# Kernel optimization log

Measured on AMD Instinct MI355X. Metric: run time of the kernel, lower is better.

## Reference

```python
import jax, jax.numpy as jnp
import numpy as np

DIM = 3072
HEADS = 24
HEAD_DIM = DIM // HEADS  # 128
B, L = 2, 2048


def setup_inputs() -> dict:
    key = jax.random.key(0)
    ks = jax.random.split(key, 6)
    x = jax.random.normal(ks[0], (B, L, DIM), dtype=jnp.float32)
    # Build a genuine rotary freqs_cis tensor: [1,1,L,D/2,2,2]
    half = HEAD_DIM // 2
    inv_freq = 1.0 / (10000.0 ** (jnp.arange(0, half, dtype=jnp.float32) / half))
    ang = jnp.arange(L, dtype=jnp.float32)[:, None] * inv_freq[None, :]  # [L, D/2]
    cos, sin = jnp.cos(ang), jnp.sin(ang)
    # rotation matrix [[cos, -sin],[sin, cos]] stacked on last two dims
    pe = jnp.stack(
        [jnp.stack([cos, -sin], axis=-1), jnp.stack([sin, cos], axis=-1)], axis=-2
    )  # [L, D/2, 2, 2]
    pe = pe[None, None]  # [1,1,L,D/2,2,2]
    Wqkv = jax.random.normal(ks[1], (3 * DIM, DIM), dtype=jnp.float32) * 0.02
    bqkv = jax.random.normal(ks[2], (3 * DIM,), dtype=jnp.float32) * 0.02
    q_scale = jnp.ones((HEAD_DIM,), dtype=jnp.float32)
    k_scale = jnp.ones((HEAD_DIM,), dtype=jnp.float32)
    Wproj = jax.random.normal(ks[3], (DIM, DIM), dtype=jnp.float32) * 0.02
    bproj = jax.random.normal(ks[4], (DIM,), dtype=jnp.float32) * 0.02
    return {"x": x, "pe": pe, "Wqkv": Wqkv, "bqkv": bqkv,
            "q_scale": q_scale, "k_scale": k_scale,
            "Wproj": Wproj, "bproj": bproj}


def _rms_norm(t, scale):
    # computed in fp32 like the torch module (eps=1e-6)
    rrms = jax.lax.rsqrt(jnp.mean(t * t, axis=-1, keepdims=True) + 1e-6)
    return t * rrms * scale


def _apply_rope(t, pe):
    # t: [B,H,L,D]; pe: [1,1,L,D/2,2,2]
    b, h, l, d = t.shape
    t2 = t.reshape(b, h, l, d // 2, 1, 2)
    out = pe[..., 0] * t2[..., 0] + pe[..., 1] * t2[..., 1]  # [B,H,L,D/2,2]
    return out.reshape(b, h, l, d)


def reference(x, pe, Wqkv, bqkv, q_scale, k_scale, Wproj, bproj):
    b, l, dim = x.shape
    d = q_scale.shape[0]
    h = dim // d
    qkv = x @ Wqkv.T + bqkv                       # [B,L,3*dim]
    qkv = qkv.reshape(b, l, 3, h, d)
    q, k, v = jnp.transpose(qkv, (2, 0, 3, 1, 4))  # each [B,H,L,D]
    q = _rms_norm(q, q_scale)
    k = _rms_norm(k, k_scale)
    q = _apply_rope(q, pe)
    k = _apply_rope(k, pe)
    scale = 1.0 / jnp.sqrt(jnp.float32(d))
    scores = jnp.einsum("bhqd,bhkd->bhqk", q, k) * scale
    attn = jax.nn.softmax(scores, axis=-1)
    out = jnp.einsum("bhqk,bhkd->bhqd", attn, v)  # [B,H,L,D]
    out = jnp.transpose(out, (0, 2, 1, 3)).reshape(b, l, h * d)
    return out @ Wproj.T + bproj
```

## Files before the change

### kernel.cpp

```cpp
#include <hip/hip_runtime.h>

#define DIM   3072
#define HEADS 24
#define HDIM  128
#define BB    2
#define LSEQ  2048
#define BL    4096
#define NQKV  9216

typedef __bf16 bf16;
typedef __bf16 bf16x8 __attribute__((ext_vector_type(8)));
typedef float  f32x4  __attribute__((ext_vector_type(4)));

__device__ __forceinline__ void async_cp16(void* lds, const void* gp) {
  __builtin_amdgcn_global_load_lds(
      (const __attribute__((address_space(1))) void*)gp,
      (__attribute__((address_space(3))) void*)lds, 16, 0, 0);
}

__global__ void sniff_dtype(const unsigned short* __restrict__ w, int* __restrict__ flag) {
  if (threadIdx.x == 0 && blockIdx.x == 0) {
    int big = 0;
    for (int i = 0; i < 64; ++i) {
      const int e = (w[i] >> 7) & 0xFF;
      if (e >= 127) ++big;
    }
    *flag = (big >= 4) ? 1 : 0;
  }
}

__global__ __launch_bounds__(256) void to_bf16(
    const void* __restrict__ src, bf16* __restrict__ dst, long n,
    const int* __restrict__ flag) {
  const bool f = (*flag != 0);
  long i = (long)blockIdx.x * blockDim.x + threadIdx.x;
  const long stride = (long)gridDim.x * blockDim.x;
  if (f) {
    const float* s = (const float*)src;
    for (; i < n; i += stride) dst[i] = (bf16)s[i];
  } else {
    const unsigned short* s = (const unsigned short*)src;
    unsigned short* d = (unsigned short*)dst;
    for (; i < n; i += stride) d[i] = s[i];
  }
}

__global__ __launch_bounds__(256) void gemm_bt_bias(
    const bf16* __restrict__ A, const bf16* __restrict__ Bw,
    const bf16* __restrict__ bias, void* __restrict__ Cv,
    int M, int N, int K, const int* __restrict__ flag)
{
  __shared__ bf16 As[128*32];
  __shared__ bf16 Bs[128*32];
  const bool f32out = (flag != nullptr) && (*flag != 0);
  const int tid  = threadIdx.x;
  const int wave = tid >> 6, lane = tid & 63;
  const int bm = blockIdx.x * 128, bn = blockIdx.y * 128;
  const int wm = (wave >> 1) * 64, wn = (wave & 1) * 64;
  const int lm = lane & 15, q8 = (lane >> 4) * 8;
  const int rsub = lane >> 2;
  const int cb   = (lane & 3) * 16;

  const f32x4 zero4 = {0.f, 0.f, 0.f, 0.f};
  f32x4 acc[4][4];
  for (int i = 0; i < 4; ++i)
    for (int j = 0; j < 4; ++j) acc[i][j] = zero4;

  for (int k0 = 0; k0 < K; k0 += 32) {
    #pragma unroll
    for (int j = 0; j < 2; ++j) {
      const int r = wave*32 + j*16 + rsub;
      async_cp16((char*)As + r*64 + cb,
                 (const char*)(A + (size_t)(bm + r)*K + k0) + cb);
      async_cp16((char*)Bs + r*64 + cb,
                 (const char*)(Bw + (size_t)(bn + r)*K + k0) + cb);
    }
    __syncthreads();
    bf16x8 af[4], bfr[4];
    #pragma unroll
    for (int t = 0; t < 4; ++t) {
      af[t]  = *(const bf16x8*)&As[(wm + t*16 + lm)*32 + q8];
      bfr[t] = *(const bf16x8*)&Bs[(wn + t*16 + lm)*32 + q8];
    }
    #pragma unroll
    for (int mt = 0; mt < 4; ++mt)
      #pragma unroll
      for (int nt = 0; nt < 4; ++nt)
        acc[mt][nt] = __builtin_amdgcn_mfma_f32_16x16x32_bf16(
            af[mt], bfr[nt], acc[mt][nt], 0, 0, 0);
    __syncthreads();
  }

  const int q = lane >> 4;
  #pragma unroll
  for (int nt = 0; nt < 4; ++nt) {
    const int col = bn + wn + nt*16 + lm;
    const float bv = (float)bias[col];
    #pragma unroll
    for (int mt = 0; mt < 4; ++mt) {
      #pragma unroll
      for (int r = 0; r < 4; ++r) {
        const int row = bm + wm + mt*16 + q*4 + r;
        const float v = acc[mt][nt][r] + bv;
        if (f32out) ((float*)Cv)[(size_t)row*N + col] = v;
        else        ((bf16*)Cv)[(size_t)row*N + col] = (bf16)v;
      }
    }
  }
}

__global__ __launch_bounds__(128) void norm_rope(
    bf16* __restrict__ qkv,
    const bf16* __restrict__ pe,
    const bf16* __restrict__ q_scale,
    const bf16* __restrict__ k_scale)
{
  const int blk = blockIdx.x;
  const int h  = blk % HEADS;
  const int bl = blk / HEADS;
  const int l  = bl & (LSEQ - 1);
  const int d  = threadIdx.x;

  bf16* row = qkv + (size_t)bl * NQKV;
  bf16* qp_ = row + h*HDIM + d;
  bf16* kp_ = row + DIM + h*HDIM + d;
  float qv = (float)*qp_;
  float kv = (float)*kp_;

  float sq = qv*qv, sk = kv*kv;
  #pragma unroll
  for (int off = 32; off >= 1; off >>= 1) {
    sq += __shfl_xor(sq, off);
    sk += __shfl_xor(sk, off);
  }
  __shared__ float red[4];
  const int wv = threadIdx.x >> 6;
  if ((threadIdx.x & 63) == 0) { red[wv*2] = sq; red[wv*2+1] = sk; }
  __syncthreads();
  const float rq = rsqrtf((red[0] + red[2]) * (1.f/HDIM) + 1e-6f);
  const float rk = rsqrtf((red[1] + red[3]) * (1.f/HDIM) + 1e-6f);

  qv = qv * rq * (float)q_scale[d];
  kv = kv * rk * (float)k_scale[d];

  const float qpn = __shfl_xor(qv, 1);
  const float kpn = __shfl_xor(kv, 1);
  const bf16* pp = pe + ((size_t)l*64 + (d >> 1))*4 + (d & 1)*2;
  const float c0 = (float)pp[0], c1 = (float)pp[1];
  const float qe = (d & 1) ? qpn : qv, qo = (d & 1) ? qv : qpn;
  const float ke = (d & 1) ? kpn : kv, ko = (d & 1) ? kv : kpn;
  float qr = c0*qe + c1*qo;
  float kr = c0*ke + c1*ko;
  qr *= 0.08838834764831845f;

  *qp_ = (bf16)qr;
  *kp_ = (bf16)kr;
}

__global__ __launch_bounds__(256) void v_transpose(
    const bf16* __restrict__ qkv, bf16* __restrict__ Vt)
{
  __shared__ bf16 tile[64][144];
  const int bid = blockIdx.x;
  const int lt = bid & 31;
  const int h  = (bid >> 5) % HEADS;
  const int b  = bid / (32*HEADS);
  const int l0 = lt * 64;
  const int tid = threadIdx.x;

  #pragma unroll
  for (int pass = 0; pass < 4; ++pass) {
    const int r = pass*16 + (tid >> 4);
    const int c = (tid & 15) * 8;
    const bf16* src = qkv + (size_t)(b*LSEQ + l0 + r)*NQKV + (2*DIM) + h*HDIM + c;
    *(uint4*)&tile[r][c] = *(const uint4*)src;
  }
  __syncthreads();
  #pragma unroll
  for (int pass = 0; pass < 4; ++pass) {
    const int d = pass*32 + (tid >> 3);
    const int c = (tid & 7) * 8;
    alignas(16) bf16 tmp[8];
    #pragma unroll
    for (int j = 0; j < 8; ++j) tmp[j] = tile[c + j][d];
    bf16* dst = Vt + (((size_t)b*HEADS + h)*HDIM + d)*LSEQ + l0 + c;
    *(uint4*)dst = *(const uint4*)tmp;
  }
}

__global__ __launch_bounds__(256, 2) void flash_attn(
    const bf16* __restrict__ qkv,
    const bf16* __restrict__ Vt,
    bf16* __restrict__ AO)
{
  extern __shared__ bf16 smem[];
  bf16* Ps = smem + 32768;

  const int bid = blockIdx.x;
  const int lt = bid & 15;
  const int h  = (bid >> 4) % HEADS;
  const int b  = bid / (16*HEADS);
  const int l0 = lt * 128;
  const int tid = threadIdx.x, wave = tid >> 6, lane = tid & 63;
  const int lm = lane & 15, quad = lane >> 4;

  const bf16* Qg = qkv + (size_t)(b*LSEQ)*NQKV + h*HDIM;
  const bf16* Kg = Qg + DIM;
  const bf16* Vg = Vt + (size_t)(b*HEADS + h)*HDIM*LSEQ;

  const int srow = lane >> 4;
  const int sg   = lane & 15;
  const int vrow = lane >> 3;
  const int vg   = lane & 7;

  #pragma unroll
  for (int j = 0; j < 8; ++j) {
    const int rl = wave*32 + j*4 + srow;
    const int g  = sg ^ (rl & 15);
    async_cp16((char*)smem + rl*256 + sg*16,
               (const char*)(Qg + (size_t)(l0 + rl)*NQKV + g*8));
  }
  __syncthreads();
  bf16x8 aq[2][4];
  #pragma unroll
  for (int half = 0; half < 2; ++half)
    #pragma unroll
    for (int ks = 0; ks < 4; ++ks)
      aq[half][ks] = *(const bf16x8*)
          &smem[(half*64 + wave*16 + lm)*128 + (((ks*4 + quad) ^ lm) * 8)];
  __syncthreads();

  const f32x4 zero4 = {0.f, 0.f, 0.f, 0.f};
  f32x4 o[2][8];
  float lp[2][4];
  #pragma unroll
  for (int s2 = 0; s2 < 2; ++s2) {
    #pragma unroll
    for (int dt = 0; dt < 8; ++dt) o[s2][dt] = zero4;
    #pragma unroll
    for (int r = 0; r < 4; ++r) lp[s2][r] = 0.f;
  }

  #pragma unroll
  for (int j = 0; j < 4; ++j) {
    const int rl = wave*16 + j*4 + srow;
    const int g  = sg ^ (rl & 15);
    async_cp16((char*)smem + rl*256 + sg*16,
               (const char*)(Kg + (size_t)rl*NQKV + g*8));
  }
  #pragma unroll
  for (int j = 0; j < 4; ++j) {
    const int dd = wave*32 + j*8 + vrow;
    const int g  = vg ^ (dd & 7);
    async_cp16((char*)smem + 32768 + dd*128 + vg*16,
               (const char*)(Vg + (size_t)dd*LSEQ + g*8));
  }

  for (int it = 0; it < LSEQ/64; ++it) {
    __syncthreads();
    const int cur = it & 1;
    if (it + 1 < LSEQ/64) {
      const int nxt = 1 - cur;
      const int kv0 = (it + 1) * 64;
      #pragma unroll
      for (int j = 0; j < 4; ++j) {
        const int rl = wave*16 + j*4 + srow;
        const int g  = sg ^ (rl & 15);
        async_cp16((char*)smem + nxt*16384 + rl*256 + sg*16,
                   (const char*)(Kg + (size_t)(kv0 + rl)*NQKV + g*8));
      }
      #pragma unroll
      for (int j = 0; j < 4; ++j) {
        const int dd = wave*32 + j*8 + vrow;
        const int g  = vg ^ (dd & 7);
        async_cp16((char*)smem + 32768 + nxt*16384 + dd*128 + vg*16,
                   (const char*)(Vg + (size_t)dd*LSEQ + kv0 + g*8));
      }
    }

    const bf16* Ksb = smem + cur*8192;
    const bf16* Vsb = smem + 16384 + cur*8192;

    f32x4 s[2][4];
    #pragma unroll
    for (int s2 = 0; s2 < 2; ++s2)
      #pragma unroll
      for (int nt = 0; nt < 4; ++nt) s[s2][nt] = zero4;
    #pragma unroll
    for (int nt = 0; nt < 4; ++nt) {
      bf16x8 bk[4];
      #pragma unroll
      for (int ks = 0; ks < 4; ++ks)
        bk[ks] = *(const bf16x8*)
            &Ksb[(nt*16 + lm)*128 + (((ks*4 + quad) ^ lm) * 8)];
      #pragma unroll
      for (int half = 0; half < 2; ++half)
        #pragma unroll
        for (int ks = 0; ks < 4; ++ks)
          s[half][nt] = __builtin_amdgcn_mfma_f32_16x16x32_bf16(
              aq[half][ks], bk[ks], s[half][nt], 0, 0, 0);
    }

    #pragma unroll
    for (int half = 0; half < 2; ++half)
      #pragma unroll
      for (int r = 0; r < 4; ++r) {
        const int pr = quad*4 + r;
        #pragma unroll
        for (int nt = 0; nt < 4; ++nt) {
          const float e = __expf(s[half][nt][r]);
          const bf16 pb = (bf16)e;
          Ps[wave*2048 + half*1024 + pr*64 +
             (((nt*2 + (lm >> 3)) ^ (pr & 7)) * 8) + (lm & 7)] = pb;
          lp[half][r] += (float)pb;
        }
      }

    #pragma unroll
    for (int ks2 = 0; ks2 < 2; ++ks2) {
      const int psl = (((ks2*4 + quad) ^ (lm & 7)) * 8);
      const bf16x8 ap0 = *(const bf16x8*)&Ps[wave*2048 +        lm*64 + psl];
      const bf16x8 ap1 = *(const bf16x8*)&Ps[wave*2048 + 1024 + lm*64 + psl];
      #pragma unroll
      for (int dt = 0; dt < 8; ++dt) {
        bf16x8 bv = *(const bf16x8*)&Vsb[(dt*16 + lm)*64 + psl];
        o[0][dt] = __builtin_amdgcn_mfma_f32_16x16x32_bf16(ap0, bv, o[0][dt], 0, 0, 0);
        o[1][dt] = __builtin_amdgcn_mfma_f32_16x16x32_bf16(ap1, bv, o[1][dt], 0, 0, 0);
      }
    }
  }

  #pragma unroll
  for (int half = 0; half < 2; ++half)
    #pragma unroll
    for (int r = 0; r < 4; ++r) {
      float v = lp[half][r];
      v += __shfl_xor(v, 1);
      v += __shfl_xor(v, 2);
      v += __shfl_xor(v, 4);
      v += __shfl_xor(v, 8);
      const float rli = 1.f / v;
      const int row = b*LSEQ + l0 + half*64 + wave*16 + quad*4 + r;
      #pragma unroll
      for (int dt = 0; dt < 8; ++dt) {
        const int col = h*HDIM + dt*16 + lm;
        AO[(size_t)row*DIM + col] = (bf16)(o[half][dt][r] * rli);
      }
    }
}

extern "C" void kernel_launch(void* const* d_in, const int* in_sizes, int n_in,
                              void* d_out, int out_size, void* d_ws, size_t ws_size,
                              hipStream_t stream)
{
  (void)in_sizes; (void)n_in; (void)out_size; (void)ws_size;
  bf16* ws = (bf16*)d_ws;
  int*  flag = (int*)d_ws;
  bf16* cx  = ws + 128;
  bf16* cWq = cx  + (size_t)BL*DIM;
  bf16* cWp = cWq + (size_t)NQKV*DIM;
  bf16* cpe = cWp + (size_t)DIM*DIM;
  bf16* cbq = cpe + (size_t)LSEQ*256;
  bf16* cbp = cbq + NQKV;
  bf16* cqs = cbp + DIM;
  bf16* cks = cqs + HDIM;
  bf16* qkv = cks + HDIM;
  bf16* Vt  = cWq;
  bf16* AO  = cx;

  static bool attr_set = false;
  if (!attr_set) {
    hipFuncSetAttribute((const void*)flash_attn,
                        hipFuncAttributeMaxDynamicSharedMemorySize, 81920);
    attr_set = true;
  }

  hipLaunchKernelGGL(sniff_dtype, dim3(1), dim3(64), 0, stream,
                     (const unsigned short*)d_in[2], flag);
  hipLaunchKernelGGL(to_bf16, dim3(4096), dim3(256), 0, stream,
                     d_in[0], cx,  (long)BL*DIM, flag);
  hipLaunchKernelGGL(to_bf16, dim3(4096), dim3(256), 0, stream,
                     d_in[2], cWq, (long)NQKV*DIM, flag);
  hipLaunchKernelGGL(to_bf16, dim3(4096), dim3(256), 0, stream,
                     d_in[6], cWp, (long)DIM*DIM, flag);
  hipLaunchKernelGGL(to_bf16, dim3(512), dim3(256), 0, stream,
                     d_in[1], cpe, (long)LSEQ*256, flag);
  hipLaunchKernelGGL(to_bf16, dim3(36), dim3(256), 0, stream,
                     d_in[3], cbq, (long)NQKV, flag);
  hipLaunchKernelGGL(to_bf16, dim3(12), dim3(256), 0, stream,
                     d_in[7], cbp, (long)DIM, flag);
  hipLaunchKernelGGL(to_bf16, dim3(1), dim3(256), 0, stream,
                     d_in[4], cqs, (long)HDIM, flag);
  hipLaunchKernelGGL(to_bf16, dim3(1), dim3(256), 0, stream,
                     d_in[5], cks, (long)HDIM, flag);

  hipLaunchKernelGGL(gemm_bt_bias, dim3(BL/128, NQKV/128), dim3(256), 0, stream,
                     cx, cWq, cbq, qkv, BL, NQKV, DIM, (const int*)nullptr);
  hipLaunchKernelGGL(norm_rope, dim3(BL*HEADS), dim3(128), 0, stream,
                     qkv, cpe, cqs, cks);
  hipLaunchKernelGGL(v_transpose, dim3(BB*HEADS*(LSEQ/64)), dim3(256), 0, stream,
                     qkv, Vt);
  hipLaunchKernelGGL(flash_attn, dim3(BB*HEADS*(LSEQ/128)), dim3(256), 81920, stream,
                     qkv, Vt, AO);
  hipLaunchKernelGGL(gemm_bt_bias, dim3(BL/128, DIM/128), dim3(256), 0, stream,
                     AO, cWp, cbp, d_out, BL, DIM, DIM, flag);
}
```

Before: 837.9 us.

## Replace GEMM with 256x256 double-buffered, swizzled, XCD-remapped MFMA kernel

Replaces the 128x128 single-buffered GEMM with a 256x256 tile kernel using 8 waves, a BK of 64, and double-buffered LDS (128 KB) filled by async global-to-LDS loads that overlap with the MFMA work. LDS is XOR-swizzled to cut bank conflicts, and workgroup IDs are remapped across the 8 XCDs to improve L2 locality. The compute is split into four phases with barriers and setprio so fragment loads interleave with MFMAs. The large LDS footprint limits occupancy, and the output projection grid gets only 192 blocks, which may underfill the CUs.

```diff
diff --git a/kernel.cpp b/kernel.cpp
--- a/kernel.cpp
+++ b/kernel.cpp
@@ -45,65 +45,164 @@
   }
 }
 
-__global__ __launch_bounds__(256) void gemm_bt_bias(
+__device__ __forceinline__ void stage_half(
+    const bf16* __restrict__ g, int ldk, int row0, int k0,
+    char* lds, int wave, int lane)
+{
+  #pragma unroll
+  for (int j = 0; j < 2; ++j) {
+    const int idx = (j*8 + wave)*64 + lane;
+    const int r   = idx >> 3;
+    const int sg  = idx & 7;
+    const int gs  = sg ^ (((r >> 2) & 1) << 1);
+    async_cp16(lds + idx*16,
+               (const char*)(g + (size_t)(row0 + r)*ldk + k0) + gs*16);
+  }
+}
+
+#define FRAG(base, row, ks) \
+  (*(const bf16x8*)((base) + (size_t)(row)*128 + \
+     (((((ks)*4) + quad) ^ ((((row) >> 2) & 1) << 1)) * 16)))
+
+__global__ __launch_bounds__(512, 2) void gemm256(
     const bf16* __restrict__ A, const bf16* __restrict__ Bw,
     const bf16* __restrict__ bias, void* __restrict__ Cv,
     int M, int N, int K, const int* __restrict__ flag)
 {
-  __shared__ bf16 As[128*32];
-  __shared__ bf16 Bs[128*32];
+  extern __shared__ char sm[];
   const bool f32out = (flag != nullptr) && (*flag != 0);
-  const int tid  = threadIdx.x;
-  const int wave = tid >> 6, lane = tid & 63;
-  const int bm = blockIdx.x * 128, bn = blockIdx.y * 128;
-  const int wm = (wave >> 1) * 64, wn = (wave & 1) * 64;
-  const int lm = lane & 15, q8 = (lane >> 4) * 8;
-  const int rsub = lane >> 2;
-  const int cb   = (lane & 3) * 16;
-
+  const int tid = threadIdx.x, wave = tid >> 6, lane = tid & 63;
+  const int lm = lane & 15, quad = lane >> 4;
+  const int wm = wave >> 2, wn = wave & 3;
+
+  const int gx = gridDim.x, nwg = gx * gridDim.y;
+  const int orig = blockIdx.y * gx + blockIdx.x;
+  const int cpx = nwg >> 3;
+  const int wg  = (orig & 7) * cpx + (orig >> 3);
+  const int bm = (wg % gx) * 256;
+  const int bn = (wg / gx) * 256;
+
+  const int KT = K >> 6;
+
+  f32x4 acc[8][4];
   const f32x4 zero4 = {0.f, 0.f, 0.f, 0.f};
-  f32x4 acc[4][4];
-  for (int i = 0; i < 4; ++i)
+  #pragma unroll
+  for (int i = 0; i < 8; ++i)
+    #pragma unroll
     for (int j = 0; j < 4; ++j) acc[i][j] = zero4;
 
-  for (int k0 = 0; k0 < K; k0 += 32) {
-    #pragma unroll
-    for (int j = 0; j < 2; ++j) {
-      const int r = wave*32 + j*16 + rsub;
-      async_cp16((char*)As + r*64 + cb,
-                 (const char*)(A + (size_t)(bm + r)*K + k0) + cb);
-      async_cp16((char*)Bs + r*64 + cb,
-                 (const char*)(Bw + (size_t)(bn + r)*K + k0) + cb);
-    }
-    __syncthreads();
-    bf16x8 af[4], bfr[4];
-    #pragma unroll
-    for (int t = 0; t < 4; ++t) {
-      af[t]  = *(const bf16x8*)&As[(wm + t*16 + lm)*32 + q8];
-      bfr[t] = *(const bf16x8*)&Bs[(wn + t*16 + lm)*32 + q8];
-    }
-    #pragma unroll
-    for (int mt = 0; mt < 4; ++mt)
-      #pragma unroll
-      for (int nt = 0; nt < 4; ++nt)
-        acc[mt][nt] = __builtin_amdgcn_mfma_f32_16x16x32_bf16(
-            af[mt], bfr[nt], acc[mt][nt], 0, 0, 0);
-    __syncthreads();
-  }
-
-  const int q = lane >> 4;
-  #pragma unroll
-  for (int nt = 0; nt < 4; ++nt) {
-    const int col = bn + wn + nt*16 + lm;
+  stage_half(A,  K, bm,       0, sm,          wave, lane);
+  stage_half(A,  K, bm + 128, 0, sm + 16384,  wave, lane);
+  stage_half(Bw, K, bn,       0, sm + 32768,  wave, lane);
+  stage_half(Bw, K, bn + 128, 0, sm + 49152,  wave, lane);
+  asm volatile("s_waitcnt vmcnt(0)" ::: "memory");
+  __builtin_amdgcn_s_barrier();
+
+  bf16x8 af[4][2], b0[2][2], b1[2][2];
+
+  for (int kt = 0; kt < KT; ++kt) {
+    const char* At = sm + (kt & 1) * 65536;
+    const char* Bt = At + 32768;
+
+    #pragma unroll
+    for (int mf = 0; mf < 4; ++mf)
+      #pragma unroll
+      for (int ks = 0; ks < 2; ++ks)
+        af[mf][ks] = FRAG(At, wm*128 + mf*16 + lm, ks);
+    #pragma unroll
+    for (int nf = 0; nf < 2; ++nf)
+      #pragma unroll
+      for (int ks = 0; ks < 2; ++ks)
+        b0[nf][ks] = FRAG(Bt, wn*64 + nf*16 + lm, ks);
+    if (kt + 1 < KT) {
+      char* dA = sm + ((kt + 1) & 1) * 65536;
+      const int k1 = (kt + 1) * 64;
+      stage_half(A,  K, bm,       k1, dA,          wave, lane);
+      stage_half(A,  K, bm + 128, k1, dA + 16384,  wave, lane);
+      stage_half(Bw, K, bn,       k1, dA + 32768,  wave, lane);
+      stage_half(Bw, K, bn + 128, k1, dA + 49152,  wave, lane);
+    }
+    __builtin_amdgcn_sched_barrier(0);
+    __builtin_amdgcn_s_barrier();
+    __builtin_amdgcn_s_setprio(1);
+    #pragma unroll
+    for (int mf = 0; mf < 4; ++mf)
+      #pragma unroll
+      for (int nf = 0; nf < 2; ++nf)
+        #pragma unroll
+        for (int ks = 0; ks < 2; ++ks)
+          acc[mf][nf] = __builtin_amdgcn_mfma_f32_16x16x32_bf16(
+              af[mf][ks], b0[nf][ks], acc[mf][nf], 0, 0, 0);
+    __builtin_amdgcn_s_setprio(0);
+    __builtin_amdgcn_sched_barrier(0);
+    __builtin_amdgcn_s_barrier();
+
+    #pragma unroll
+    for (int nf = 0; nf < 2; ++nf)
+      #pragma unroll
+      for (int ks = 0; ks < 2; ++ks)
+        b1[nf][ks] = FRAG(Bt, wn*64 + 32 + nf*16 + lm, ks);
+    __builtin_amdgcn_sched_barrier(0);
+    __builtin_amdgcn_s_barrier();
+    __builtin_amdgcn_s_setprio(1);
+    #pragma unroll
+    for (int mf = 0; mf < 4; ++mf)
+      #pragma unroll
+      for (int nf = 0; nf < 2; ++nf)
+        #pragma unroll
+        for (int ks = 0; ks < 2; ++ks)
+          acc[mf][2 + nf] = __builtin_amdgcn_mfma_f32_16x16x32_bf16(
+              af[mf][ks], b1[nf][ks], acc[mf][2 + nf], 0, 0, 0);
+    __builtin_amdgcn_s_setprio(0);
+    __builtin_amdgcn_sched_barrier(0);
+    __builtin_amdgcn_s_barrier();
+
+    #pragma unroll
+    for (int mf = 0; mf < 4; ++mf)
+      #pragma unroll
+      for (int ks = 0; ks < 2; ++ks)
+        af[mf][ks] = FRAG(At, wm*128 + 64 + mf*16 + lm, ks);
+    __builtin_amdgcn_sched_barrier(0);
+    __builtin_amdgcn_s_barrier();
+    __builtin_amdgcn_s_setprio(1);
+    #pragma unroll
+    for (int mf = 0; mf < 4; ++mf)
+      #pragma unroll
+      for (int nf = 0; nf < 2; ++nf)
+        #pragma unroll
+        for (int ks = 0; ks < 2; ++ks)
+          acc[4 + mf][2 + nf] = __builtin_amdgcn_mfma_f32_16x16x32_bf16(
+              af[mf][ks], b1[nf][ks], acc[4 + mf][2 + nf], 0, 0, 0);
+    __builtin_amdgcn_s_setprio(0);
+    __builtin_amdgcn_sched_barrier(0);
+    __builtin_amdgcn_s_barrier();
+
+    __builtin_amdgcn_s_setprio(1);
+    #pragma unroll
+    for (int mf = 0; mf < 4; ++mf)
+      #pragma unroll
+      for (int nf = 0; nf < 2; ++nf)
+        #pragma unroll
+        for (int ks = 0; ks < 2; ++ks)
+          acc[4 + mf][nf] = __builtin_amdgcn_mfma_f32_16x16x32_bf16(
+              af[mf][ks], b0[nf][ks], acc[4 + mf][nf], 0, 0, 0);
+    __builtin_amdgcn_s_setprio(0);
+    asm volatile("s_waitcnt vmcnt(0)" ::: "memory");
+    __builtin_amdgcn_s_barrier();
+  }
+
+  #pragma unroll
+  for (int ni = 0; ni < 4; ++ni) {
+    const int col = bn + wn*64 + ni*16 + lm;
     const float bv = (float)bias[col];
     #pragma unroll
-    for (int mt = 0; mt < 4; ++mt) {
+    for (int mi = 0; mi < 8; ++mi) {
+      const int row0 = bm + wm*128 + mi*16 + quad*4;
       #pragma unroll
       for (int r = 0; r < 4; ++r) {
-        const int row = bm + wm + mt*16 + q*4 + r;
-        const float v = acc[mt][nt][r] + bv;
-        if (f32out) ((float*)Cv)[(size_t)row*N + col] = v;
-        else        ((bf16*)Cv)[(size_t)row*N + col] = (bf16)v;
+        const float v = acc[mi][ni][r] + bv;
+        if (f32out) ((float*)Cv)[(size_t)(row0 + r)*N + col] = v;
+        else        ((bf16*)Cv)[(size_t)(row0 + r)*N + col] = (bf16)v;
       }
     }
   }
@@ -372,6 +471,8 @@
   if (!attr_set) {
     hipFuncSetAttribute((const void*)flash_attn,
                         hipFuncAttributeMaxDynamicSharedMemorySize, 81920);
+    hipFuncSetAttribute((const void*)gemm256,
+                        hipFuncAttributeMaxDynamicSharedMemorySize, 131072);
     attr_set = true;
   }
 
@@ -394,7 +495,7 @@
   hipLaunchKernelGGL(to_bf16, dim3(1), dim3(256), 0, stream,
                      d_in[5], cks, (long)HDIM, flag);
 
-  hipLaunchKernelGGL(gemm_bt_bias, dim3(BL/128, NQKV/128), dim3(256), 0, stream,
+  hipLaunchKernelGGL(gemm256, dim3(BL/256, NQKV/256), dim3(512), 131072, stream,
                      cx, cWq, cbq, qkv, BL, NQKV, DIM, (const int*)nullptr);
   hipLaunchKernelGGL(norm_rope, dim3(BL*HEADS), dim3(128), 0, stream,
                      qkv, cpe, cqs, cks);
@@ -402,6 +503,6 @@
                      qkv, Vt);
   hipLaunchKernelGGL(flash_attn, dim3(BB*HEADS*(LSEQ/128)), dim3(256), 81920, stream,
                      qkv, Vt, AO);
-  hipLaunchKernelGGL(gemm_bt_bias, dim3(BL/128, DIM/128), dim3(256), 0, stream,
+  hipLaunchKernelGGL(gemm256, dim3(BL/256, DIM/256), dim3(512), 131072, stream,
                      AO, cWp, cbp, d_out, BL, DIM, DIM, flag);
 }
```

New measurement: 826.1 us. No clear change (-1.4%).
